# Performance work log

Measured on AMD Instinct MI355X. Metric: run time of the kernel, lower is better.

## Reference

```python
import jax, jax.numpy as jnp
import numpy as np

N_EMBD = 1024  # C in forward; scale uses C**-0.5

def setup_inputs() -> dict:
    key = jax.random.key(0)
    k1, k2, k3, k4 = jax.random.split(key, 4)
    B, T, C, H = 4, 4096, N_EMBD, 64
    x = jax.random.normal(k1, (B, T, C), dtype=jnp.float32)
    # nn.Linear weights stored already-transposed as [in, out] for x @ W
    s = 1.0 / np.sqrt(C)
    Wq = jax.random.normal(k2, (C, H), dtype=jnp.float32) * s
    Wk = jax.random.normal(k3, (C, H), dtype=jnp.float32) * s
    Wv = jax.random.normal(k4, (C, H), dtype=jnp.float32) * s
    return {"x": x, "Wq": Wq, "Wk": Wk, "Wv": Wv}

def reference(x, Wq, Wk, Wv):
    B, T, C = x.shape
    q = jnp.einsum('btc,ch->bth', x, Wq)
    k = jnp.einsum('btc,ch->bth', x, Wk)
    v = jnp.einsum('btc,ch->bth', x, Wv)
    # scores scaled by C**-0.5 (note: original scales by embed dim, not head_size)
    wei = jnp.einsum('bth,bsh->bts', q, k) * (C ** -0.5)
    causal = jnp.tril(jnp.ones((T, T), dtype=bool))  # [T,T]
    wei = jnp.where(causal[None, :, :], wei, -jnp.inf)
    wei = jax.nn.softmax(wei, axis=-1)
    # dropout p=0.0 (eval-mode reference): identity
    out = jnp.einsum('bts,bsh->bth', wei, v)
    return out
```

## Files before the change

### kernel.cpp

```cpp
#include <hip/hip_runtime.h>

typedef __bf16 bf16x8 __attribute__((ext_vector_type(8)));
typedef float floatx16 __attribute__((ext_vector_type(16)));
typedef float floatx4 __attribute__((ext_vector_type(4)));

#define T_ 4096
#define STK 72
#define NSPB 144

#define WT_OFF 0u
#define Q_OFF  393216u
#define K_OFF  2490368u
#define V_OFF  4587520u
#define OP_OFF 6684672u
#define ML_OFF 25559040u

__device__ __forceinline__ unsigned short bf16bits(float f) {
  __bf16 h = (__bf16)f;
  return __builtin_bit_cast(unsigned short, h);
}

__global__ void wprep(const float* __restrict__ Wq, const float* __restrict__ Wk,
                      const float* __restrict__ Wv, __bf16* __restrict__ Wtg) {
  int idx = blockIdx.x * 256 + threadIdx.x;
  int mat = idx >> 16;
  int r = idx & 65535;
  int h = r & 63;
  int k = r >> 6;
  const float* W = (mat == 0) ? Wq : ((mat == 1) ? Wk : Wv);
  float v = W[k * 64 + h];
  if (mat == 0) v *= 0.03125f * 1.4426950408889634f;
  Wtg[(size_t)(mat * 64 + h) * 1024 + k] = (__bf16)v;
}

__global__ __launch_bounds__(256, 3) void proj(const float* __restrict__ x,
                                               const __bf16* __restrict__ Wtg,
                                               __bf16* __restrict__ Qp,
                                               __bf16* __restrict__ Kp,
                                               __bf16* __restrict__ Vp) {
  __shared__ __align__(16) unsigned short sm[(64 + 192) * STK];
  unsigned short* xt = sm;
  unsigned short* wt = sm + 64 * STK;
  const int tid = threadIdx.x;
  const int wave = tid >> 6, lane = tid & 63;
  const int l15 = lane & 15, quad = lane >> 4;
  const size_t row0 = (size_t)blockIdx.x * 64;

  floatx4 acc[3][4];
#pragma unroll
  for (int m = 0; m < 3; m++)
#pragma unroll
    for (int t = 0; t < 4; t++)
#pragma unroll
      for (int i = 0; i < 4; i++) acc[m][t][i] = 0.0f;

  for (int kc = 0; kc < 16; ++kc) {
    __syncthreads();
    {
      int row = tid >> 2, seg = tid & 3;
      const float* src = x + (row0 + row) * 1024 + kc * 64 + seg * 16;
      float f[16];
      *(float4*)(f) = *(const float4*)(src);
      *(float4*)(f + 4) = *(const float4*)(src + 4);
      *(float4*)(f + 8) = *(const float4*)(src + 8);
      *(float4*)(f + 12) = *(const float4*)(src + 12);
      unsigned short hb[16];
#pragma unroll
      for (int i = 0; i < 16; i++) hb[i] = bf16bits(f[i]);
      *(uint4*)&xt[row * STK + seg * 16] = *(uint4*)(hb);
      *(uint4*)&xt[row * STK + seg * 16 + 8] = *(uint4*)(hb + 8);
    }
#pragma unroll
    for (int i = 0; i < 6; i++) {
      int idx = tid + 256 * i;
      int r = idx >> 3, c = (idx & 7) * 8;
      *(uint4*)&wt[r * STK + c] = *(const uint4*)(Wtg + (size_t)r * 1024 + kc * 64 + c);
    }
    __syncthreads();
#pragma unroll
    for (int ks = 0; ks < 2; ++ks) {
      bf16x8 a = *(const bf16x8*)&xt[(wave * 16 + l15) * STK + ks * 32 + quad * 8];
#pragma unroll
      for (int m = 0; m < 3; m++)
#pragma unroll
        for (int ht = 0; ht < 4; ++ht) {
          bf16x8 b = *(const bf16x8*)&wt[(m * 64 + ht * 16 + l15) * STK + ks * 32 + quad * 8];
          acc[m][ht] = __builtin_amdgcn_mfma_f32_16x16x32_bf16(a, b, acc[m][ht], 0, 0, 0);
        }
    }
  }
#pragma unroll
  for (int m = 0; m < 3; m++) {
    __bf16* outp = (m == 0) ? Qp : ((m == 1) ? Kp : Vp);
#pragma unroll
    for (int ht = 0; ht < 4; ++ht)
#pragma unroll
      for (int r = 0; r < 4; r++) {
        size_t row = row0 + wave * 16 + quad * 4 + r;
        outp[row * 64 + ht * 16 + l15] = (__bf16)acc[m][ht][r];
      }
  }
}

__global__ __launch_bounds__(256, 3) void attn1(const __bf16* __restrict__ Qp,
                                                const __bf16* __restrict__ Kp,
                                                const __bf16* __restrict__ Vp,
                                                float* __restrict__ Opart,
                                                float* __restrict__ mlpart) {
  __shared__ __align__(16) unsigned char smraw[36864];
  unsigned short* Kl = (unsigned short*)smraw;
  unsigned short* Vtl = Kl + 64 * STK;
  unsigned short* Pl = Vtl + 64 * STK;
  float* Oe = (float*)smraw;

  const int tid = threadIdx.x;
  const int wave = tid >> 6, lane = tid & 63;
  const int l31 = lane & 31, half = lane >> 5;

  const int bid = blockIdx.x;
  const int b = bid / NSPB;
  const int f = bid - b * NSPB;
  int qt = 0, cum = 0;
  for (;;) { int s = (qt + 4) >> 2; if (f < cum + s) break; cum += s; qt++; }
  const int si = f - cum;
  const int S = (qt + 4) >> 2;
  const int n_iters = 2 * (qt + 1);
  const int bbase = n_iters / S, rem = n_iters % S;
  const int it0 = si * bbase + (si < rem ? si : rem);
  const int it1 = it0 + bbase + (si < rem ? 1 : 0);

  const int qb = qt * 128;
  const size_t brow = (size_t)b * 4096;

  bf16x8 qf[4];
  {
    const __bf16* qptr = Qp + (brow + qb + wave * 32 + l31) * 64 + half * 8;
#pragma unroll
    for (int ks = 0; ks < 4; ks++) qf[ks] = *(const bf16x8*)(qptr + ks * 16);
  }

  floatx16 o0, o1;
#pragma unroll
  for (int r = 0; r < 16; r++) { o0[r] = 0.0f; o1[r] = 0.0f; }
  float m_run = -1e30f, l_run = 0.0f;
  unsigned short* Pw = Pl + wave * 32 * STK;
  const int qrow = qb + wave * 32 + l31;

  for (int it = it0; it < it1; ++it) {
    const int k0 = it * 64;
#pragma unroll
    for (int i = 0; i < 2; i++) {
      int u = tid + 256 * i;
      int kr = u >> 3, c = (u & 7) * 8;
      *(uint4*)&Kl[kr * STK + c] = *(const uint4*)(Kp + (brow + k0 + kr) * 64 + c);
    }
    {
      int kp = tid & 31, h0 = ((tid >> 5) & 7) * 8;
      const __bf16* vp = Vp + (brow + k0 + 2 * kp) * 64 + h0;
      unsigned short va[8], vb[8];
      *(uint4*)va = *(const uint4*)(vp);
      *(uint4*)vb = *(const uint4*)(vp + 64);
#pragma unroll
      for (int j = 0; j < 8; j++) {
        unsigned int w = (unsigned int)va[j] | ((unsigned int)vb[j] << 16);
        *(unsigned int*)&Vtl[(h0 + j) * STK + 2 * kp] = w;
      }
    }
    __syncthreads();
    floatx16 s0, s1;
#pragma unroll
    for (int r = 0; r < 16; r++) { s0[r] = 0.0f; s1[r] = 0.0f; }
#pragma unroll
    for (int ks = 0; ks < 4; ks++) {
      bf16x8 ka = *(const bf16x8*)&Kl[l31 * STK + ks * 16 + half * 8];
      bf16x8 kb = *(const bf16x8*)&Kl[(32 + l31) * STK + ks * 16 + half * 8];
      s0 = __builtin_amdgcn_mfma_f32_32x32x16_bf16(ka, qf[ks], s0, 0, 0, 0);
      s1 = __builtin_amdgcn_mfma_f32_32x32x16_bf16(kb, qf[ks], s1, 0, 0, 0);
    }
    if (k0 + 64 > qb) {
#pragma unroll
      for (int r = 0; r < 16; r++) {
        int rs = (r & 3) + 8 * (r >> 2) + 4 * half;
        if (k0 + rs > qrow) s0[r] = -1e30f;
        if (k0 + 32 + rs > qrow) s1[r] = -1e30f;
      }
    }
    float pm = -1e30f;
#pragma unroll
    for (int r = 0; r < 16; r++) { pm = fmaxf(pm, s0[r]); pm = fmaxf(pm, s1[r]); }
    pm = fmaxf(pm, __shfl_xor(pm, 32));
    float m_new = fmaxf(m_run, pm);
    float alpha = __builtin_amdgcn_exp2f(m_run - m_new);
    float psum = 0.0f;
#pragma unroll
    for (int r = 0; r < 16; r++) {
      s0[r] = __builtin_amdgcn_exp2f(s0[r] - m_new);
      s1[r] = __builtin_amdgcn_exp2f(s1[r] - m_new);
      psum += s0[r] + s1[r];
    }
    psum += __shfl_xor(psum, 32);
    l_run = l_run * alpha + psum;
    m_run = m_new;
#pragma unroll
    for (int r = 0; r < 16; r++) { o0[r] *= alpha; o1[r] *= alpha; }
#pragma unroll
    for (int g = 0; g < 4; ++g) {
      int kb0 = 8 * g + 4 * half;
      unsigned int w0 = (unsigned int)bf16bits(s0[4 * g]) | ((unsigned int)bf16bits(s0[4 * g + 1]) << 16);
      unsigned int w1 = (unsigned int)bf16bits(s0[4 * g + 2]) | ((unsigned int)bf16bits(s0[4 * g + 3]) << 16);
      *(uint2*)&Pw[l31 * STK + kb0] = make_uint2(w0, w1);
      unsigned int w2 = (unsigned int)bf16bits(s1[4 * g]) | ((unsigned int)bf16bits(s1[4 * g + 1]) << 16);
      unsigned int w3 = (unsigned int)bf16bits(s1[4 * g + 2]) | ((unsigned int)bf16bits(s1[4 * g + 3]) << 16);
      *(uint2*)&Pw[l31 * STK + 32 + kb0] = make_uint2(w2, w3);
    }
#pragma unroll
    for (int kst = 0; kst < 4; ++kst) {
      bf16x8 pf = *(const bf16x8*)&Pw[l31 * STK + kst * 16 + half * 8];
      bf16x8 va = *(const bf16x8*)&Vtl[l31 * STK + kst * 16 + half * 8];
      bf16x8 vb = *(const bf16x8*)&Vtl[(32 + l31) * STK + kst * 16 + half * 8];
      o0 = __builtin_amdgcn_mfma_f32_32x32x16_bf16(va, pf, o0, 0, 0, 0);
      o1 = __builtin_amdgcn_mfma_f32_32x32x16_bf16(vb, pf, o1, 0, 0, 0);
    }
    __syncthreads();
  }
#pragma unroll
  for (int r = 0; r < 16; r++) {
    int rs = (r & 3) + 8 * (r >> 2) + 4 * half;
    Oe[(wave * 32 + l31) * 68 + rs] = o0[r];
    Oe[(wave * 32 + l31) * 68 + 32 + rs] = o1[r];
  }
  if (lane < 32) {
    mlpart[(size_t)bid * 256 + wave * 32 + l31] = m_run;
    mlpart[(size_t)bid * 256 + 128 + wave * 32 + l31] = l_run;
  }
  __syncthreads();
  {
    float* dst = Opart + (size_t)bid * 8192;
    int r = tid >> 1, hh = (tid & 1) * 32;
#pragma unroll
    for (int i = 0; i < 8; i++)
      *(float4*)&dst[r * 64 + hh + 4 * i] = *(float4*)&Oe[r * 68 + hh + 4 * i];
  }
}

__global__ __launch_bounds__(256, 4) void attn2(const float* __restrict__ Opart,
                                                const float* __restrict__ mlpart,
                                                float* __restrict__ out) {
  const int bid = blockIdx.x;
  const int b = bid >> 7, rg = bid & 127;
  const int qt = rg >> 2;
  int cum = 0;
  for (int i = 0; i < qt; i++) cum += (i + 4) >> 2;
  const int S = (qt + 4) >> 2;
  const int t = threadIdx.x;
  const int r = t >> 3;
  const int prow = (rg & 3) * 32 + r;
  const int h0 = (t & 7) * 8;

  float M = -1e30f;
  for (int s = 0; s < S; s++)
    M = fmaxf(M, mlpart[(size_t)(b * NSPB + cum + s) * 256 + prow]);
  float a[8];
#pragma unroll
  for (int i = 0; i < 8; i++) a[i] = 0.0f;
  float L = 0.0f;
  for (int s = 0; s < S; s++) {
    size_t pb = (size_t)(b * NSPB + cum + s);
    float w = __builtin_amdgcn_exp2f(mlpart[pb * 256 + prow] - M);
    L += w * mlpart[pb * 256 + 128 + prow];
    const float* op = Opart + pb * 8192 + prow * 64 + h0;
    float4 v0 = *(const float4*)op;
    float4 v1 = *(const float4*)(op + 4);
    a[0] += w * v0.x; a[1] += w * v0.y; a[2] += w * v0.z; a[3] += w * v0.w;
    a[4] += w * v1.x; a[5] += w * v1.y; a[6] += w * v1.z; a[7] += w * v1.w;
  }
  float inv = 1.0f / L;
  float* po = out + ((size_t)b * 4096 + rg * 32 + r) * 64 + h0;
  float4 r0, r1;
  r0.x = a[0] * inv; r0.y = a[1] * inv; r0.z = a[2] * inv; r0.w = a[3] * inv;
  r1.x = a[4] * inv; r1.y = a[5] * inv; r1.z = a[6] * inv; r1.w = a[7] * inv;
  *(float4*)po = r0;
  *(float4*)(po + 4) = r1;
}

extern "C" void kernel_launch(void* const* d_in, const int* in_sizes, int n_in,
                              void* d_out, int out_size, void* d_ws, size_t ws_size,
                              hipStream_t stream) {
  (void)in_sizes; (void)n_in; (void)out_size; (void)ws_size;
  const float* x = (const float*)d_in[0];
  const float* Wq = (const float*)d_in[1];
  const float* Wk = (const float*)d_in[2];
  const float* Wv = (const float*)d_in[3];
  char* ws = (char*)d_ws;
  __bf16* Wtg = (__bf16*)(ws + WT_OFF);
  __bf16* Qp = (__bf16*)(ws + Q_OFF);
  __bf16* Kp = (__bf16*)(ws + K_OFF);
  __bf16* Vp = (__bf16*)(ws + V_OFF);
  float* Opart = (float*)(ws + OP_OFF);
  float* mlp = (float*)(ws + ML_OFF);
  float* out = (float*)d_out;

  hipLaunchKernelGGL(wprep, dim3(768), dim3(256), 0, stream, Wq, Wk, Wv, Wtg);
  hipLaunchKernelGGL(proj, dim3(256), dim3(256), 0, stream, x, Wtg, Qp, Kp, Vp);
  hipLaunchKernelGGL(attn1, dim3(4 * NSPB), dim3(256), 0, stream, Qp, Kp, Vp, Opart, mlp);
  hipLaunchKernelGGL(attn2, dim3(512), dim3(256), 0, stream, Opart, mlp, out);
}
```

Before: 172.1 us.

## Halve projection row tile to double block count and split waves 2x2

The projection kernel now processes 32 rows per block instead of 64, which doubles the grid from 256 to 512 blocks so more of the GPU's compute units have work. The four waves are rearranged into a 2x2 grid, each computing 16 rows by 96 output columns across Q/K/V. Launch bounds go up to 4 blocks per SM. In exchange, the weight tile is loaded into shared memory twice as often in total, because it is reloaded per block while each block covers fewer rows.

```diff
diff --git a/kernel.cpp b/kernel.cpp
--- a/kernel.cpp
+++ b/kernel.cpp
@@ -33,42 +33,38 @@
   Wtg[(size_t)(mat * 64 + h) * 1024 + k] = (__bf16)v;
 }
 
-__global__ __launch_bounds__(256, 3) void proj(const float* __restrict__ x,
+__global__ __launch_bounds__(256, 4) void proj(const float* __restrict__ x,
                                                const __bf16* __restrict__ Wtg,
                                                __bf16* __restrict__ Qp,
                                                __bf16* __restrict__ Kp,
                                                __bf16* __restrict__ Vp) {
-  __shared__ __align__(16) unsigned short sm[(64 + 192) * STK];
+  __shared__ __align__(16) unsigned short sm[(32 + 192) * STK];
   unsigned short* xt = sm;
-  unsigned short* wt = sm + 64 * STK;
+  unsigned short* wt = sm + 32 * STK;
   const int tid = threadIdx.x;
   const int wave = tid >> 6, lane = tid & 63;
+  const int wm = wave & 1, wn = wave >> 1;
   const int l15 = lane & 15, quad = lane >> 4;
-  const size_t row0 = (size_t)blockIdx.x * 64;
-
-  floatx4 acc[3][4];
-#pragma unroll
-  for (int m = 0; m < 3; m++)
-#pragma unroll
-    for (int t = 0; t < 4; t++)
-#pragma unroll
-      for (int i = 0; i < 4; i++) acc[m][t][i] = 0.0f;
+  const size_t row0 = (size_t)blockIdx.x * 32;
+
+  floatx4 acc[6];
+#pragma unroll
+  for (int t = 0; t < 6; t++)
+#pragma unroll
+    for (int i = 0; i < 4; i++) acc[t][i] = 0.0f;
 
   for (int kc = 0; kc < 16; ++kc) {
     __syncthreads();
     {
-      int row = tid >> 2, seg = tid & 3;
-      const float* src = x + (row0 + row) * 1024 + kc * 64 + seg * 16;
-      float f[16];
+      int row = tid >> 3, seg = tid & 7;
+      const float* src = x + (row0 + row) * 1024 + kc * 64 + seg * 8;
+      float f[8];
       *(float4*)(f) = *(const float4*)(src);
       *(float4*)(f + 4) = *(const float4*)(src + 4);
-      *(float4*)(f + 8) = *(const float4*)(src + 8);
-      *(float4*)(f + 12) = *(const float4*)(src + 12);
-      unsigned short hb[16];
-#pragma unroll
-      for (int i = 0; i < 16; i++) hb[i] = bf16bits(f[i]);
-      *(uint4*)&xt[row * STK + seg * 16] = *(uint4*)(hb);
-      *(uint4*)&xt[row * STK + seg * 16 + 8] = *(uint4*)(hb + 8);
+      unsigned short hb[8];
+#pragma unroll
+      for (int i = 0; i < 8; i++) hb[i] = bf16bits(f[i]);
+      *(uint4*)&xt[row * STK + seg * 8] = *(uint4*)(hb);
     }
 #pragma unroll
     for (int i = 0; i < 6; i++) {
@@ -79,26 +75,24 @@
     __syncthreads();
 #pragma unroll
     for (int ks = 0; ks < 2; ++ks) {
-      bf16x8 a = *(const bf16x8*)&xt[(wave * 16 + l15) * STK + ks * 32 + quad * 8];
-#pragma unroll
-      for (int m = 0; m < 3; m++)
-#pragma unroll
-        for (int ht = 0; ht < 4; ++ht) {
-          bf16x8 b = *(const bf16x8*)&wt[(m * 64 + ht * 16 + l15) * STK + ks * 32 + quad * 8];
-          acc[m][ht] = __builtin_amdgcn_mfma_f32_16x16x32_bf16(a, b, acc[m][ht], 0, 0, 0);
-        }
-    }
-  }
-#pragma unroll
-  for (int m = 0; m < 3; m++) {
-    __bf16* outp = (m == 0) ? Qp : ((m == 1) ? Kp : Vp);
-#pragma unroll
-    for (int ht = 0; ht < 4; ++ht)
-#pragma unroll
-      for (int r = 0; r < 4; r++) {
-        size_t row = row0 + wave * 16 + quad * 4 + r;
-        outp[row * 64 + ht * 16 + l15] = (__bf16)acc[m][ht][r];
+      bf16x8 a = *(const bf16x8*)&xt[(wm * 16 + l15) * STK + ks * 32 + quad * 8];
+#pragma unroll
+      for (int ht = 0; ht < 6; ++ht) {
+        bf16x8 b = *(const bf16x8*)&wt[(wn * 96 + ht * 16 + l15) * STK + ks * 32 + quad * 8];
+        acc[ht] = __builtin_amdgcn_mfma_f32_16x16x32_bf16(a, b, acc[ht], 0, 0, 0);
       }
+    }
+  }
+#pragma unroll
+  for (int ht = 0; ht < 6; ++ht) {
+    int g0 = wn * 96 + ht * 16;
+    int mat = g0 >> 6, h0 = g0 & 63;
+    __bf16* outp = (mat == 0) ? Qp : ((mat == 1) ? Kp : Vp);
+#pragma unroll
+    for (int r = 0; r < 4; r++) {
+      size_t row = row0 + wm * 16 + quad * 4 + r;
+      outp[row * 64 + h0 + l15] = (__bf16)acc[ht][r];
+    }
   }
 }
 
@@ -301,7 +295,7 @@
   float* out = (float*)d_out;
 
   hipLaunchKernelGGL(wprep, dim3(768), dim3(256), 0, stream, Wq, Wk, Wv, Wtg);
-  hipLaunchKernelGGL(proj, dim3(256), dim3(256), 0, stream, x, Wtg, Qp, Kp, Vp);
+  hipLaunchKernelGGL(proj, dim3(512), dim3(256), 0, stream, x, Wtg, Qp, Kp, Vp);
   hipLaunchKernelGGL(attn1, dim3(4 * NSPB), dim3(256), 0, stream, Qp, Kp, Vp, Opart, mlp);
   hipLaunchKernelGGL(attn2, dim3(512), dim3(256), 0, stream, Opart, mlp, out);
 }
```

Measured after the change: 148.9 us. -13.5%, faster.
